# Performance work log

Measured on AMD Instinct MI355X. Metric: run time of the kernel, lower is better.

## Reference

```python
import jax, jax.numpy as jnp
import numpy as np

NUM_STEPS = 5  # DVF2DDF(num_steps=5)


def _warp(vol, ddf, mode):
    """MONAI Warp: sample vol at (voxel index + ddf), align_corners=True, zeros padding.
    vol: [N,C,D,H,W]; ddf: [N,3,D,H,W] (channels = d,h,w displacement)."""
    N, C, D, H, W = vol.shape
    gd, gh, gw = jnp.meshgrid(jnp.arange(D, dtype=ddf.dtype),
                              jnp.arange(H, dtype=ddf.dtype),
                              jnp.arange(W, dtype=ddf.dtype), indexing='ij')
    cd = gd + ddf[:, 0]  # [N,D,H,W] absolute sample coords
    ch = gh + ddf[:, 1]
    cw = gw + ddf[:, 2]
    vol_flat = vol.reshape(N, C, D * H * W)

    def gather(di, hi, wi, valid):
        dc = jnp.clip(di, 0, D - 1)
        hc = jnp.clip(hi, 0, H - 1)
        wc = jnp.clip(wi, 0, W - 1)
        flat = ((dc * H + hc) * W + wc).reshape(N, 1, -1)
        v = jnp.take_along_axis(vol_flat, flat, axis=2).reshape(N, C, D, H, W)
        return v * valid[:, None]

    def in_bounds(di, hi, wi):
        return ((di >= 0) & (di < D) & (hi >= 0) & (hi < H)
                & (wi >= 0) & (wi < W)).astype(vol.dtype)

    if mode == 'nearest':
        di = jnp.round(cd).astype(jnp.int32)
        hi = jnp.round(ch).astype(jnp.int32)
        wi = jnp.round(cw).astype(jnp.int32)
        return gather(di, hi, wi, in_bounds(di, hi, wi))

    # trilinear ('bilinear' in grid_sample naming)
    d0 = jnp.floor(cd); h0 = jnp.floor(ch); w0 = jnp.floor(cw)
    fd = cd - d0; fh = ch - h0; fw = cw - w0
    d0i = d0.astype(jnp.int32); h0i = h0.astype(jnp.int32); w0i = w0.astype(jnp.int32)
    out = jnp.zeros_like(vol)
    for dd in (0, 1):
        for dh in (0, 1):
            for dw in (0, 1):
                di = d0i + dd; hi = h0i + dh; wi = w0i + dw
                wgt = ((fd if dd else 1 - fd)
                       * (fh if dh else 1 - fh)
                       * (fw if dw else 1 - fw))
                out = out + gather(di, hi, wi, in_bounds(di, hi, wi)) * wgt[:, None]
    return out


def _dvf2ddf(dvf, num_steps=NUM_STEPS):
    """Scaling-and-squaring integration of a stationary velocity field (MONAI DVF2DDF)."""
    ddf = dvf / (2 ** num_steps)
    for _ in range(num_steps):
        ddf = ddf + _warp(ddf, ddf, 'bilinear')
    return ddf


def setup_inputs() -> dict:
    key = jax.random.key(0)
    ks = jax.random.split(key, 6)
    D = H = W = 160
    return {
        "dvf0": jax.random.normal(ks[0], (1, 3, D, H, W), jnp.float32),
        "dvf1": jax.random.normal(ks[1], (1, 3, D, H, W), jnp.float32),
        "image": jax.random.normal(ks[2], (1, 1, D, H, W), jnp.float32),
        "cavity": jax.random.randint(ks[3], (1, 1, D, H, W), 0, 5, jnp.int32),
        "coronary": jax.random.randint(ks[4], (1, 1, D, H, W), 0, 3, jnp.int32),
        "w": jax.random.uniform(ks[5], (), jnp.float32),
    }


def reference(dvf0, dvf1, image, cavity, coronary, w):
    # linear blend of the two neighbouring phase DVFs
    dvf = dvf0 * (1 - w) + dvf1 * w
    ddf = _dvf2ddf(dvf)
    img_warped = _warp(image, ddf, 'bilinear')
    # labels are concatenated along batch and warped with nearest, ddf repeated
    labels = jnp.concatenate([cavity, coronary], axis=0).astype(jnp.float32)  # [2,1,D,H,W]
    lab_warped = _warp(labels, jnp.tile(ddf, (2, 1, 1, 1, 1)), 'nearest')
    cav_warped = lab_warped[0][None].astype(jnp.uint8)
    cor_warped = lab_warped[1][None].astype(jnp.uint8)
    return img_warped, cav_warped, cor_warped, ddf
```

## Files before the change

### kernel.cpp

```cpp
#include <hip/hip_runtime.h>

#define DD 160
#define HH 160
#define WW 160
#define PL (HH*WW)
#define S (DD*PL)

__device__ __forceinline__ float fmul(float a, float b){ return __fmul_rn(a,b); }
__device__ __forceinline__ float fadd(float a, float b){ return __fadd_rn(a,b); }
__device__ __forceinline__ float fsub(float a, float b){ return __fsub_rn(a,b); }

__global__ __launch_bounds__(256) void init_kernel(const float* __restrict__ dvf0,
                                                   const float* __restrict__ dvf1,
                                                   const float* __restrict__ wp,
                                                   float* __restrict__ outi) {
    int p = (blockIdx.x * 256 + threadIdx.x) * 4;
    float w = wp[0];
    float onew = fsub(1.0f, w);
    float a0[4], a1[4], a2[4], b0[4], b1[4], b2[4];
    *(float4*)a0 = *(const float4*)(dvf0 + p);
    *(float4*)a1 = *(const float4*)(dvf0 + S + p);
    *(float4*)a2 = *(const float4*)(dvf0 + 2 * S + p);
    *(float4*)b0 = *(const float4*)(dvf1 + p);
    *(float4*)b1 = *(const float4*)(dvf1 + S + p);
    *(float4*)b2 = *(const float4*)(dvf1 + 2 * S + p);
    float o[12];
    #pragma unroll
    for (int j = 0; j < 4; ++j) {
        o[3*j]   = fmul(fadd(fmul(a0[j], onew), fmul(b0[j], w)), 0.03125f);
        o[3*j+1] = fmul(fadd(fmul(a1[j], onew), fmul(b1[j], w)), 0.03125f);
        o[3*j+2] = fmul(fadd(fmul(a2[j], onew), fmul(b2[j], w)), 0.03125f);
    }
    float* dst = outi + (size_t)3 * p;
    *(float4*)(dst)     = *(float4*)(o);
    *(float4*)(dst + 4) = *(float4*)(o + 4);
    *(float4*)(dst + 8) = *(float4*)(o + 8);
}

template<bool PLANAR>
__global__ __launch_bounds__(256) void warp_step(const float* __restrict__ in,
                                                 float* __restrict__ out) {
    int b  = (blockIdx.x & 7) * 1000 + (blockIdx.x >> 3);
    int ix = b % 5;
    int r  = b / 5;
    int iy = r % 20;
    int iz = r / 20;
    int lane = threadIdx.x & 63, wid = threadIdx.x >> 6;
    int x  = (ix << 5) | (lane & 31);
    int y  = (iy << 3) | (wid << 1) | (lane >> 5);
    int z0 = iz << 1;
    int p0 = (z0 * HH + y) * WW + x;

    float ctr[2][3];
    #pragma unroll
    for (int j = 0; j < 2; ++j) {
        const float* src = in + (size_t)3 * (p0 + j * PL);
        ctr[j][0] = src[0]; ctr[j][1] = src[1]; ctr[j][2] = src[2];
    }

    #pragma unroll
    for (int j = 0; j < 2; ++j) {
        int z = z0 + j;
        int p = p0 + j * PL;
        float vd = ctr[j][0], vh = ctr[j][1], vw = ctr[j][2];
        float cd = fadd((float)z, vd);
        float ch = fadd((float)y, vh);
        float cw = fadd((float)x, vw);

        float d0 = floorf(cd), h0 = floorf(ch), w0 = floorf(cw);
        float fd = fsub(cd, d0), fh = fsub(ch, h0), fw = fsub(cw, w0);
        float gd = fsub(1.0f, fd), gh = fsub(1.0f, fh), gw = fsub(1.0f, fw);
        int d0i = (int)d0, h0i = (int)h0, w0i = (int)w0;

        int   qa[8];
        float wt[8];
        #pragma unroll
        for (int t = 0; t < 8; ++t) {
            int dd = t >> 2, dh = (t >> 1) & 1, dw = t & 1;
            int di = d0i + dd, hi = h0i + dh, wi = w0i + dw;
            bool valid = (di >= 0) & (di < DD) & (hi >= 0) & (hi < HH)
                       & (wi >= 0) & (wi < WW);
            float wgt = fmul(fmul(dd ? fd : gd, dh ? fh : gh), dw ? fw : gw);
            wt[t] = valid ? wgt : 0.0f;
            int dc = min(max(di, 0), DD - 1);
            int hc = min(max(hi, 0), HH - 1);
            int wc = min(max(wi, 0), WW - 1);
            qa[t] = 3 * ((dc * HH + hc) * WW + wc);
        }
        float g[8][3];
        #pragma unroll
        for (int t = 0; t < 8; ++t) {
            g[t][0] = in[qa[t]];
            g[t][1] = in[qa[t] + 1];
            g[t][2] = in[qa[t] + 2];
        }
        float acc0 = 0.0f, acc1 = 0.0f, acc2 = 0.0f;
        #pragma unroll
        for (int t = 0; t < 8; ++t) {
            acc0 = fadd(acc0, fmul(g[t][0], wt[t]));
            acc1 = fadd(acc1, fmul(g[t][1], wt[t]));
            acc2 = fadd(acc2, fmul(g[t][2], wt[t]));
        }
        float r0 = fadd(vd, acc0);
        float r1 = fadd(vh, acc1);
        float r2 = fadd(vw, acc2);

        if (PLANAR) {
            out[p] = r0; out[S + p] = r1; out[2 * S + p] = r2;
        } else {
            float* dst = out + (size_t)3 * p;
            dst[0] = r0; dst[1] = r1; dst[2] = r2;
        }
    }
}

__global__ __launch_bounds__(256) void final_kernel(const float* __restrict__ ddf,
                                                    const float* __restrict__ image,
                                                    const int* __restrict__ cav,
                                                    const int* __restrict__ cor,
                                                    float* __restrict__ out) {
    int b  = (blockIdx.x & 7) * 1000 + (blockIdx.x >> 3);
    int ix = b % 5;
    int r  = b / 5;
    int iy = r % 20;
    int iz = r / 20;
    int lane = threadIdx.x & 63, wid = threadIdx.x >> 6;
    int x  = (ix << 5) | (lane & 31);
    int y  = (iy << 3) | (wid << 1) | (lane >> 5);
    int z0 = iz << 1;
    int p0 = (z0 * HH + y) * WW + x;

    float dzs[2], dhs[2], dws[2];
    #pragma unroll
    for (int j = 0; j < 2; ++j) {
        dzs[j] = ddf[p0 + j * PL];
        dhs[j] = ddf[S + p0 + j * PL];
        dws[j] = ddf[2 * S + p0 + j * PL];
    }

    #pragma unroll
    for (int j = 0; j < 2; ++j) {
        int z = z0 + j;
        int p = p0 + j * PL;
        float cd = fadd((float)z, dzs[j]);
        float ch = fadd((float)y, dhs[j]);
        float cw = fadd((float)x, dws[j]);

        float d0 = floorf(cd), h0 = floorf(ch), w0 = floorf(cw);
        float fd = fsub(cd, d0), fh = fsub(ch, h0), fw = fsub(cw, w0);
        float gd = fsub(1.0f, fd), gh = fsub(1.0f, fh), gw = fsub(1.0f, fw);
        int d0i = (int)d0, h0i = (int)h0, w0i = (int)w0;

        int   qa[8];
        float wt[8];
        #pragma unroll
        for (int t = 0; t < 8; ++t) {
            int dd = t >> 2, dh = (t >> 1) & 1, dw = t & 1;
            int di = d0i + dd, hi = h0i + dh, wi = w0i + dw;
            bool valid = (di >= 0) & (di < DD) & (hi >= 0) & (hi < HH)
                       & (wi >= 0) & (wi < WW);
            float wgt = fmul(fmul(dd ? fd : gd, dh ? fh : gh), dw ? fw : gw);
            wt[t] = valid ? wgt : 0.0f;
            int dc = min(max(di, 0), DD - 1);
            int hc = min(max(hi, 0), HH - 1);
            int wc = min(max(wi, 0), WW - 1);
            qa[t] = (dc * HH + hc) * WW + wc;
        }
        float g[8];
        #pragma unroll
        for (int t = 0; t < 8; ++t) g[t] = image[qa[t]];
        float acc = 0.0f;
        #pragma unroll
        for (int t = 0; t < 8; ++t) acc = fadd(acc, fmul(g[t], wt[t]));
        out[p] = acc;

        int di = (int)rintf(cd), hi = (int)rintf(ch), wi = (int)rintf(cw);
        bool valid = (di >= 0) & (di < DD) & (hi >= 0) & (hi < HH)
                   & (wi >= 0) & (wi < WW);
        int dc = min(max(di, 0), DD - 1);
        int hc = min(max(hi, 0), HH - 1);
        int wc = min(max(wi, 0), WW - 1);
        int q = (dc * HH + hc) * WW + wc;
        out[S + p]     = valid ? (float)cav[q] : 0.0f;
        out[2 * S + p] = valid ? (float)cor[q] : 0.0f;
    }
}

extern "C" void kernel_launch(void* const* d_in, const int* in_sizes, int n_in,
                              void* d_out, int out_size, void* d_ws, size_t ws_size,
                              hipStream_t stream) {
    const float* dvf0   = (const float*)d_in[0];
    const float* dvf1   = (const float*)d_in[1];
    const float* image  = (const float*)d_in[2];
    const int*   cav    = (const int*)d_in[3];
    const int*   cor    = (const int*)d_in[4];
    const float* w      = (const float*)d_in[5];

    float* out  = (float*)d_out;
    float* bufA = out;
    float* bufB = out + (size_t)3 * S;

    init_kernel<<<4000, 256, 0, stream>>>(dvf0, dvf1, w, bufA);
    warp_step<false><<<8000, 256, 0, stream>>>(bufA, bufB);
    warp_step<false><<<8000, 256, 0, stream>>>(bufB, bufA);
    warp_step<false><<<8000, 256, 0, stream>>>(bufA, bufB);
    warp_step<false><<<8000, 256, 0, stream>>>(bufB, bufA);
    warp_step<true ><<<8000, 256, 0, stream>>>(bufA, bufB);
    final_kernel<<<8000, 256, 0, stream>>>(bufB, image, cav, cor, bufA);
}
```

Before: 416.0 us.

## Split ddf into interleaved DH pairs plus planar W, add interior fast path

The intermediate displacement field changes from a 3-float interleaved layout to an interleaved d/h float2 array plus a separate planar w array. Each gather then becomes one aligned 8-byte load plus one 4-byte load instead of three scalar loads. The final kernel also gains an interior fast path that skips per-corner clamping and validity masks when all eight trilinear corners are in bounds. The trade-offs are more loads landing on two separate memory regions and added branch divergence at the volume borders.

Measured after the change: 509.4 us. 1.22x slower.

```diff
diff --git a/kernel.cpp b/kernel.cpp
--- a/kernel.cpp
+++ b/kernel.cpp
@@ -10,10 +10,11 @@
 __device__ __forceinline__ float fadd(float a, float b){ return __fadd_rn(a,b); }
 __device__ __forceinline__ float fsub(float a, float b){ return __fsub_rn(a,b); }
 
+
 __global__ __launch_bounds__(256) void init_kernel(const float* __restrict__ dvf0,
                                                    const float* __restrict__ dvf1,
                                                    const float* __restrict__ wp,
-                                                   float* __restrict__ outi) {
+                                                   float* __restrict__ outb) {
     int p = (blockIdx.x * 256 + threadIdx.x) * 4;
     float w = wp[0];
     float onew = fsub(1.0f, w);
@@ -24,22 +25,24 @@
     *(float4*)b0 = *(const float4*)(dvf1 + p);
     *(float4*)b1 = *(const float4*)(dvf1 + S + p);
     *(float4*)b2 = *(const float4*)(dvf1 + 2 * S + p);
-    float o[12];
+    float odh[8], ow[4];
     #pragma unroll
     for (int j = 0; j < 4; ++j) {
-        o[3*j]   = fmul(fadd(fmul(a0[j], onew), fmul(b0[j], w)), 0.03125f);
-        o[3*j+1] = fmul(fadd(fmul(a1[j], onew), fmul(b1[j], w)), 0.03125f);
-        o[3*j+2] = fmul(fadd(fmul(a2[j], onew), fmul(b2[j], w)), 0.03125f);
-    }
-    float* dst = outi + (size_t)3 * p;
-    *(float4*)(dst)     = *(float4*)(o);
-    *(float4*)(dst + 4) = *(float4*)(o + 4);
-    *(float4*)(dst + 8) = *(float4*)(o + 8);
+        odh[2*j]   = fmul(fadd(fmul(a0[j], onew), fmul(b0[j], w)), 0.03125f);
+        odh[2*j+1] = fmul(fadd(fmul(a1[j], onew), fmul(b1[j], w)), 0.03125f);
+        ow[j]      = fmul(fadd(fmul(a2[j], onew), fmul(b2[j], w)), 0.03125f);
+    }
+    float* dstDH = outb + (size_t)2 * p;
+    *(float4*)(dstDH)     = *(float4*)(odh);
+    *(float4*)(dstDH + 4) = *(float4*)(odh + 4);
+    *(float4*)(outb + (size_t)2 * S + p) = *(float4*)(ow);
 }
 
 template<bool PLANAR>
 __global__ __launch_bounds__(256) void warp_step(const float* __restrict__ in,
                                                  float* __restrict__ out) {
+    const float* inDH = in;
+    const float* inW  = in + (size_t)2 * S;
     int b  = (blockIdx.x & 7) * 1000 + (blockIdx.x >> 3);
     int ix = b % 5;
     int r  = b / 5;
@@ -51,18 +54,19 @@
     int z0 = iz << 1;
     int p0 = (z0 * HH + y) * WW + x;
 
-    float ctr[2][3];
-    #pragma unroll
-    for (int j = 0; j < 2; ++j) {
-        const float* src = in + (size_t)3 * (p0 + j * PL);
-        ctr[j][0] = src[0]; ctr[j][1] = src[1]; ctr[j][2] = src[2];
+    float cd_[2], ch_[2], cw_[2];
+    #pragma unroll
+    for (int j = 0; j < 2; ++j) {
+        int pc = p0 + j * PL;
+        float2 t = *(const float2*)(inDH + (size_t)2 * pc);
+        cd_[j] = t.x; ch_[j] = t.y; cw_[j] = inW[pc];
     }
 
     #pragma unroll
     for (int j = 0; j < 2; ++j) {
         int z = z0 + j;
         int p = p0 + j * PL;
-        float vd = ctr[j][0], vh = ctr[j][1], vw = ctr[j][2];
+        float vd = cd_[j], vh = ch_[j], vw = cw_[j];
         float cd = fadd((float)z, vd);
         float ch = fadd((float)y, vh);
         float cw = fadd((float)x, vw);
@@ -85,21 +89,21 @@
             int dc = min(max(di, 0), DD - 1);
             int hc = min(max(hi, 0), HH - 1);
             int wc = min(max(wi, 0), WW - 1);
-            qa[t] = 3 * ((dc * HH + hc) * WW + wc);
-        }
-        float g[8][3];
+            qa[t] = (dc * HH + hc) * WW + wc;
+        }
+        float g0[8], g1[8], g2[8];
         #pragma unroll
         for (int t = 0; t < 8; ++t) {
-            g[t][0] = in[qa[t]];
-            g[t][1] = in[qa[t] + 1];
-            g[t][2] = in[qa[t] + 2];
+            float2 t2 = *(const float2*)(inDH + (size_t)2 * qa[t]);
+            g0[t] = t2.x; g1[t] = t2.y;
+            g2[t] = inW[qa[t]];
         }
         float acc0 = 0.0f, acc1 = 0.0f, acc2 = 0.0f;
         #pragma unroll
         for (int t = 0; t < 8; ++t) {
-            acc0 = fadd(acc0, fmul(g[t][0], wt[t]));
-            acc1 = fadd(acc1, fmul(g[t][1], wt[t]));
-            acc2 = fadd(acc2, fmul(g[t][2], wt[t]));
+            acc0 = fadd(acc0, fmul(g0[t], wt[t]));
+            acc1 = fadd(acc1, fmul(g1[t], wt[t]));
+            acc2 = fadd(acc2, fmul(g2[t], wt[t]));
         }
         float r0 = fadd(vd, acc0);
         float r1 = fadd(vh, acc1);
@@ -108,8 +112,9 @@
         if (PLANAR) {
             out[p] = r0; out[S + p] = r1; out[2 * S + p] = r2;
         } else {
-            float* dst = out + (size_t)3 * p;
-            dst[0] = r0; dst[1] = r1; dst[2] = r2;
+            float2* dst = (float2*)(out + (size_t)2 * p);
+            *dst = make_float2(r0, r1);
+            out[(size_t)2 * S + p] = r2;
         }
     }
 }
@@ -151,38 +156,64 @@
         float gd = fsub(1.0f, fd), gh = fsub(1.0f, fh), gw = fsub(1.0f, fw);
         int d0i = (int)d0, h0i = (int)h0, w0i = (int)w0;
 
-        int   qa[8];
-        float wt[8];
-        #pragma unroll
-        for (int t = 0; t < 8; ++t) {
-            int dd = t >> 2, dh = (t >> 1) & 1, dw = t & 1;
-            int di = d0i + dd, hi = h0i + dh, wi = w0i + dw;
+        bool fast = ((unsigned)d0i < (unsigned)(DD - 1))
+                  & ((unsigned)h0i < (unsigned)(HH - 1))
+                  & ((unsigned)w0i < (unsigned)(WW - 1));
+        if (fast) {
+            const float* bp0 = image + (d0i * HH + h0i) * WW + w0i;
+            const float* bp1 = bp0 + PL;
+            float g[8];
+            g[0] = bp0[0];      g[1] = bp0[1];
+            g[2] = bp0[WW];     g[3] = bp0[WW + 1];
+            g[4] = bp1[0];      g[5] = bp1[1];
+            g[6] = bp1[WW];     g[7] = bp1[WW + 1];
+            float w00 = fmul(gd, gh), w01 = fmul(gd, fh);
+            float w10 = fmul(fd, gh), w11 = fmul(fd, fh);
+            float wt[8] = { fmul(w00, gw), fmul(w00, fw), fmul(w01, gw), fmul(w01, fw),
+                            fmul(w10, gw), fmul(w10, fw), fmul(w11, gw), fmul(w11, fw) };
+            float acc = 0.0f;
+            #pragma unroll
+            for (int t = 0; t < 8; ++t) acc = fadd(acc, fmul(g[t], wt[t]));
+            out[p] = acc;
+
+            int di = (int)rintf(cd), hi = (int)rintf(ch), wi = (int)rintf(cw);
+            int q = (di * HH + hi) * WW + wi;
+            out[S + p]     = (float)cav[q];
+            out[2 * S + p] = (float)cor[q];
+        } else {
+            int   qa[8];
+            float wt[8];
+            #pragma unroll
+            for (int t = 0; t < 8; ++t) {
+                int dd = t >> 2, dh = (t >> 1) & 1, dw = t & 1;
+                int di = d0i + dd, hi = h0i + dh, wi = w0i + dw;
+                bool valid = (di >= 0) & (di < DD) & (hi >= 0) & (hi < HH)
+                           & (wi >= 0) & (wi < WW);
+                float wgt = fmul(fmul(dd ? fd : gd, dh ? fh : gh), dw ? fw : gw);
+                wt[t] = valid ? wgt : 0.0f;
+                int dc = min(max(di, 0), DD - 1);
+                int hc = min(max(hi, 0), HH - 1);
+                int wc = min(max(wi, 0), WW - 1);
+                qa[t] = (dc * HH + hc) * WW + wc;
+            }
+            float g[8];
+            #pragma unroll
+            for (int t = 0; t < 8; ++t) g[t] = image[qa[t]];
+            float acc = 0.0f;
+            #pragma unroll
+            for (int t = 0; t < 8; ++t) acc = fadd(acc, fmul(g[t], wt[t]));
+            out[p] = acc;
+
+            int di = (int)rintf(cd), hi = (int)rintf(ch), wi = (int)rintf(cw);
             bool valid = (di >= 0) & (di < DD) & (hi >= 0) & (hi < HH)
                        & (wi >= 0) & (wi < WW);
-            float wgt = fmul(fmul(dd ? fd : gd, dh ? fh : gh), dw ? fw : gw);
-            wt[t] = valid ? wgt : 0.0f;
             int dc = min(max(di, 0), DD - 1);
             int hc = min(max(hi, 0), HH - 1);
             int wc = min(max(wi, 0), WW - 1);
-            qa[t] = (dc * HH + hc) * WW + wc;
-        }
-        float g[8];
-        #pragma unroll
-        for (int t = 0; t < 8; ++t) g[t] = image[qa[t]];
-        float acc = 0.0f;
-        #pragma unroll
-        for (int t = 0; t < 8; ++t) acc = fadd(acc, fmul(g[t], wt[t]));
-        out[p] = acc;
-
-        int di = (int)rintf(cd), hi = (int)rintf(ch), wi = (int)rintf(cw);
-        bool valid = (di >= 0) & (di < DD) & (hi >= 0) & (hi < HH)
-                   & (wi >= 0) & (wi < WW);
-        int dc = min(max(di, 0), DD - 1);
-        int hc = min(max(hi, 0), HH - 1);
-        int wc = min(max(wi, 0), WW - 1);
-        int q = (dc * HH + hc) * WW + wc;
-        out[S + p]     = valid ? (float)cav[q] : 0.0f;
-        out[2 * S + p] = valid ? (float)cor[q] : 0.0f;
+            int q = (dc * HH + hc) * WW + wc;
+            out[S + p]     = valid ? (float)cav[q] : 0.0f;
+            out[2 * S + p] = valid ? (float)cor[q] : 0.0f;
+        }
     }
 }
 
```
